# Optimization experiments

Measured on AMD Instinct MI355X. Metric: run time of the kernel, lower is better.

Reference implementation:

```python
import jax, jax.numpy as jnp
import numpy as np

B, S, D_IN = 2, 2048, 1024
DIM, H, G = 64, 16, 4  # head dim, num_heads, kv groups


def setup_inputs() -> dict:
    key = jax.random.key(0)
    ks = jax.random.split(key, 9)
    query = jax.random.normal(ks[0], (B, S, D_IN), dtype=jnp.float32)
    key_t = jax.random.normal(ks[1], (B, S, D_IN), dtype=jnp.float32)
    value = jax.random.normal(ks[2], (B, S, D_IN), dtype=jnp.float32)
    # causal mask; masked_fill where mask == 0
    mask = jnp.tril(jnp.ones((S, S), dtype=jnp.int32))[None]  # [1,S,S]
    sc = 1.0 / np.sqrt(D_IN)
    Wq = jax.random.normal(ks[3], (H, D_IN, DIM), dtype=jnp.float32) * sc
    bq = jnp.zeros((H, DIM), dtype=jnp.float32)
    Wk = jax.random.normal(ks[4], (G, D_IN, DIM), dtype=jnp.float32) * sc
    bk = jnp.zeros((G, DIM), dtype=jnp.float32)
    Wv = jax.random.normal(ks[5], (G, D_IN, DIM), dtype=jnp.float32) * sc
    bv = jnp.zeros((G, DIM), dtype=jnp.float32)
    return {"query": query, "key": key_t, "value": value, "mask": mask,
            "Wq": Wq, "bq": bq, "Wk": Wk, "bk": bk, "Wv": Wv, "bv": bv}


def reference(query, key, value, mask, Wq, bq, Wk, bk, Wv, bv):
    # batched per-head projections (replaces the Python loop over heads)
    Q = jnp.einsum('bsd,hde->bhse', query, Wq) + bq[None, :, None, :]   # [B,H,S,E]
    K = jnp.einsum('bsd,gde->bgse', key, Wk) + bk[None, :, None, :]     # [B,G,S,E]
    V = jnp.einsum('bsd,gde->bgse', value, Wv) + bv[None, :, None, :]   # [B,G,S,E]
    # head i uses KV group i % G (as in the original loop)
    g_idx = jnp.arange(H) % G
    Kh = K[:, g_idx]  # [B,H,S,E]
    Vh = V[:, g_idx]
    attn = jnp.einsum('bhqe,bhke->bhqk', Q, Kh) / np.sqrt(DIM)          # [B,H,S,S]
    attn = jnp.where(mask[:, None] == 0, jnp.float32(-1e9), attn)
    p = jax.nn.softmax(attn, axis=-1)
    z = jnp.einsum('bhqk,bhke->bhqe', p, Vh)                             # [B,H,S,E]
    # concat heads along last dim (same order as torch.cat of z_list)
    return z.transpose(0, 2, 1, 3).reshape(B, S, H * DIM)
```

## Files before the change

### kernel.cpp

```cpp
#include <hip/hip_runtime.h>
#include <hip/hip_bf16.h>
#include <math.h>

#define S_LEN 2048
#define DIN   1024
#define NH    16
#define NG    4

typedef short s16x8 __attribute__((ext_vector_type(8)));
typedef float f32x4 __attribute__((ext_vector_type(4)));

__device__ __forceinline__ unsigned short f2bf(float x) {
  union { float f; unsigned u; } v; v.f = x;
  unsigned r = v.u + 0x7FFFu + ((v.u >> 16) & 1u);
  return (unsigned short)(r >> 16);
}
__device__ __forceinline__ unsigned cvtpk(float a, float b) {
  unsigned r;
  asm("v_cvt_pk_bf16_f32 %0, %1, %2" : "=v"(r) : "v"(a), "v"(b));
  return r;
}

#define GLOAD_LDS16(gsrc, ldst)                                              \
  __builtin_amdgcn_global_load_lds(                                         \
      (const __attribute__((address_space(1))) unsigned int*)(gsrc),        \
      (__attribute__((address_space(3))) unsigned int*)(ldst), 16, 0, 0)


__global__ __launch_bounds__(256) void k_cast(
    const float* __restrict__ q, const float* __restrict__ k,
    const float* __restrict__ v, unsigned short* __restrict__ AF) {
  __shared__ __align__(16) unsigned short L[16][264];
  const int i = blockIdx.y;
  const float* src = (i == 0) ? q : (i == 1) ? k : v;
  unsigned short* dst = AF + (size_t)i * 4194304;
  const int x = blockIdx.x;
  const int b = x >> 9, s16 = (x >> 2) & 127, dblk = x & 3;
  const int t = threadIdx.x;
  const float* base = src + ((size_t)(b * 2048 + s16 * 16)) * 1024 + dblk * 256;

  #pragma unroll
  for (int c = 0; c < 4; ++c) {
    const int idx = c * 256 + t;
    const int row = idx >> 6, c4 = (idx & 63) * 4;
    float4 xv = *(const float4*)(base + (size_t)row * 1024 + c4);
    *(uint2*)&L[row][c4] = make_uint2(cvtpk(xv.x, xv.y), cvtpk(xv.z, xv.w));
  }
  __syncthreads();

  const int w = t >> 6, l = t & 63;
  const int row = l & 15, kk = l >> 4;
  #pragma unroll
  for (int p = 0; p < 2; ++p) {
    const int dk = w * 2 + p;
    const s16x8 vreg = *(const s16x8*)&L[row][dk * 32 + kk * 8];
    unsigned short* op = dst
        + (size_t)((b * 128 + s16) * 32 + dblk * 8 + dk) * 512 + l * 8;
    *(s16x8*)op = vreg;
  }
}

__global__ __launch_bounds__(256) void k_wtrans(
    const float* __restrict__ Wq, const float* __restrict__ Wk,
    const float* __restrict__ Wv, unsigned short* __restrict__ WF) {
  __shared__ __align__(16) unsigned short T[64][72];
  const int u = blockIdx.x >> 4, D0 = (blockIdx.x & 15) * 64;
  const int t = threadIdx.x;
  const float* src = (u < 16) ? (Wq + (size_t)u * 65536)
                   : (u < 20) ? (Wk + (size_t)(u - 16) * 65536)
                              : (Wv + (size_t)(u - 20) * 65536);
  const int e4 = (t & 15) * 4, dl = t >> 4;
  #pragma unroll
  for (int p = 0; p < 4; ++p) {
    const int d = p * 16 + dl;
    float4 v = *(const float4*)(src + (size_t)(D0 + d) * 64 + e4);
    T[e4 + 0][d] = f2bf(v.x); T[e4 + 1][d] = f2bf(v.y);
    T[e4 + 2][d] = f2bf(v.z); T[e4 + 3][d] = f2bf(v.w);
  }
  __syncthreads();
  const int j = t & 7;
  #pragma unroll
  for (int p = 0; p < 2; ++p) {
    const int e = p * 32 + (t >> 3);
    unsigned short* dst = WF + (size_t)u * 65536
        + (size_t)((e >> 4) * 32 + (D0 >> 5) + (j >> 2)) * 512
        + (e & 15) * 8 + (j & 3) * 128;
    *(s16x8*)dst = *(const s16x8*)&T[e][j * 8];
  }
}

__global__ __launch_bounds__(256, 4) void k_project(
    const unsigned short* __restrict__ AF,
    const float* __restrict__ bq, const float* __restrict__ bk,
    const float* __restrict__ bv,
    const unsigned short* __restrict__ WF,
    unsigned short* __restrict__ QF,
    unsigned short* __restrict__ KF,
    unsigned short* __restrict__ VF) {
  const int i = blockIdx.x;
  const int lid = (i & 7) * 96 + (i >> 3);
  const int strip = lid / 48;
  const int rr = lid % 48;
  const int b = rr / 24, u = rr % 24;
  const int tid = threadIdx.x;
  const int w = tid >> 6, lane = tid & 63, lq = lane & 15, gq = lane >> 4;

  const unsigned short* AFp = AF
      + (size_t)((u < 16) ? 0 : (u < 20) ? 1 : 2) * 4194304
      + (size_t)b * 2097152;
  const float* bias = (u < 16) ? bq + u * 64
                    : (u < 20) ? bk + (u - 16) * 64 : bv + (u - 20) * 64;
  const unsigned short* WFp = WF + (size_t)u * 65536;
  const int sb0 = strip * 8 + w * 2;
  const float OSC = (u < 16) ? 0.1803368801111204f : 1.0f;

  f32x4 acc[2][4] = {};
  s16x8 aE[2], bE[4], aO[2], bO[4];

  auto LD = [&](s16x8 (&a)[2], s16x8 (&bf)[4], int dk) {
    a[0] = *(const s16x8*)(AFp + (size_t)((sb0 + 0) * 32 + dk) * 512 + lane * 8);
    a[1] = *(const s16x8*)(AFp + (size_t)((sb0 + 1) * 32 + dk) * 512 + lane * 8);
    #pragma unroll
    for (int n = 0; n < 4; ++n)
      bf[n] = *(const s16x8*)(WFp + (size_t)(n * 32 + dk) * 512 + lane * 8);
  };
  auto FM = [&](const s16x8 (&a)[2], const s16x8 (&bf)[4]) {
    #pragma unroll
    for (int rf = 0; rf < 2; ++rf)
      #pragma unroll
      for (int n = 0; n < 4; ++n)
        acc[rf][n] = __builtin_amdgcn_mfma_f32_16x16x32_bf16(a[rf], bf[n], acc[rf][n], 0, 0, 0);
  };

  LD(aE, bE, 0);
  for (int dk = 0; dk < 32; dk += 2) {
    LD(aO, bO, dk + 1);
    FM(aE, bE);
    if (dk + 2 < 32) LD(aE, bE, dk + 2);
    FM(aO, bO);
  }

  float bvv[4];
  #pragma unroll
  for (int n = 0; n < 4; ++n) bvv[n] = bias[n * 16 + lq];

  unsigned short* dst = (u < 16) ? QF + (size_t)(b * 16 + u) * 131072
                      : (u < 20) ? KF + (size_t)(b * 4 + (u - 16)) * 131072
                                 : VF + (size_t)(b * 4 + (u - 20)) * 131072;
  #pragma unroll
  for (int rf = 0; rf < 2; ++rf)
    #pragma unroll
    for (int n = 0; n < 4; ++n)
      #pragma unroll
      for (int r = 0; r < 4; ++r) {
        const int s = strip * 128 + w * 32 + rf * 16 + gq * 4 + r;
        const int d = n * 16 + lq;
        const unsigned short hv = f2bf((acc[rf][n][r] + bvv[n]) * OSC);
        if (u < 20)
          dst[(size_t)((s >> 4) * 2 + (d >> 5)) * 512
              + (s & 15) * 8 + ((d >> 3) & 3) * 128 + (d & 7)] = hv;
        else
          dst[(size_t)(n * 64 + (s >> 5)) * 512
              + lq * 8 + ((s >> 3) & 3) * 128 + (s & 7)] = hv;
      }
}

__global__ __launch_bounds__(256) void k_attn(
    const unsigned short* __restrict__ QF, const unsigned short* __restrict__ KF,
    const unsigned short* __restrict__ VF, float* __restrict__ out) {
  __shared__ __align__(16) unsigned short KV[2][8192];
  __shared__ __align__(16) unsigned short P[4][16][72];
  const int tid = threadIdx.x;
  const int w = tid >> 6, lane = tid & 63, lq = lane & 15, gq = lane >> 4;
  const int x = blockIdx.x;
  const int xcd = x & 7, li = x >> 3;
  const int g = xcd & 3;
  const int j = 127 - (li * 2 + (xcd >> 2));
  const int h = g + 4 * w;
  const int b = blockIdx.y;

  const unsigned short* QFp = QF + (size_t)(b * NH + h) * 131072;
  const unsigned short* KFp = KF + (size_t)(b * NG + g) * 131072;
  const unsigned short* VFp = VF + (size_t)(b * NG + g) * 131072;
  const int nt = (j >> 2) + 1;

  const s16x8 qf0 = *(const s16x8*)(QFp + (size_t)(j * 2 + 0) * 512 + lane * 8);
  const s16x8 qf1 = *(const s16x8*)(QFp + (size_t)(j * 2 + 1) * 512 + lane * 8);
  f32x4 z[4] = {};
  float lsum = 0.f;

  auto stage = [&](int t, int buf) {
    const unsigned short* ks = KFp + (size_t)t * 4096 + (w * 2) * 512 + lane * 8;
    unsigned short* kd = &KV[buf][(w * 2) * 512];
    GLOAD_LDS16(ks, kd);
    GLOAD_LDS16(ks + 512, kd + 512);
    const unsigned short* vs = VFp + (size_t)(w * 64 + t * 2) * 512 + lane * 8;
    unsigned short* vd = &KV[buf][4096 + (w * 2) * 512];
    GLOAD_LDS16(vs, vd);
    GLOAD_LDS16(vs + 512, vd + 512);
  };

  auto tile = [&](int t, int buf) {
    const unsigned short* kb = &KV[buf][0];
    const unsigned short* vb = &KV[buf][4096];
    f32x4 sv[4];
    __builtin_amdgcn_s_setprio(1);
    #pragma unroll
    for (int f = 0; f < 4; ++f) {
      const s16x8 kA = *(const s16x8*)(kb + (f * 2 + 0) * 512 + lane * 8);
      const s16x8 kB = *(const s16x8*)(kb + (f * 2 + 1) * 512 + lane * 8);
      f32x4 s = {};
      s = __builtin_amdgcn_mfma_f32_16x16x32_bf16(kA, qf0, s, 0, 0, 0);
      s = __builtin_amdgcn_mfma_f32_16x16x32_bf16(kB, qf1, s, 0, 0, 0);
      sv[f] = s;
    }
    __builtin_amdgcn_s_setprio(0);
    if (t == nt - 1) {
      const int k0 = t * 64;
      const int qrow = j * 16 + lq;
      #pragma unroll
      for (int f = 0; f < 4; ++f)
        #pragma unroll
        for (int r = 0; r < 4; ++r)
          if (k0 + f * 16 + gq * 4 + r > qrow) sv[f][r] = -1e30f;
    }
    float s0 = 0.f, s1 = 0.f;
    #pragma unroll
    for (int f = 0; f < 4; ++f) {
      float p0 = __builtin_amdgcn_exp2f(sv[f][0]);
      float p1 = __builtin_amdgcn_exp2f(sv[f][1]);
      float p2 = __builtin_amdgcn_exp2f(sv[f][2]);
      float p3 = __builtin_amdgcn_exp2f(sv[f][3]);
      s0 += p0 + p1; s1 += p2 + p3;
      *(uint2*)&P[w][lq][f * 16 + gq * 4] = make_uint2(cvtpk(p0, p1), cvtpk(p2, p3));
    }
    lsum += s0 + s1;
    const s16x8 pa0 = *(const s16x8*)&P[w][lq][gq * 8];
    const s16x8 pa1 = *(const s16x8*)&P[w][lq][32 + gq * 8];
    __builtin_amdgcn_s_setprio(1);
    #pragma unroll
    for (int n = 0; n < 4; ++n) {
      const s16x8 v0 = *(const s16x8*)(vb + (n * 2 + 0) * 512 + lane * 8);
      const s16x8 v1 = *(const s16x8*)(vb + (n * 2 + 1) * 512 + lane * 8);
      z[n] = __builtin_amdgcn_mfma_f32_16x16x32_bf16(pa0, v0, z[n], 0, 0, 0);
      z[n] = __builtin_amdgcn_mfma_f32_16x16x32_bf16(pa1, v1, z[n], 0, 0, 0);
    }
    __builtin_amdgcn_s_setprio(0);
  };

  stage(0, 0);
  asm volatile("s_waitcnt vmcnt(0)");
  __syncthreads();
  int buf = 0;
  for (int t = 0; t < nt; ++t) {
    if (t + 1 < nt) stage(t + 1, buf ^ 1);
    tile(t, buf);
    asm volatile("s_waitcnt vmcnt(0)");
    __syncthreads();
    buf ^= 1;
  }

  lsum += __shfl_xor(lsum, 16);
  lsum += __shfl_xor(lsum, 32);
  float* outp = out + (size_t)b * S_LEN * 1024 + h * 64;
  #pragma unroll
  for (int r = 0; r < 4; ++r) {
    float lr = __shfl(lsum, gq * 4 + r, 64);
    float inv = __builtin_amdgcn_rcpf(lr);
    float* op = outp + (size_t)(j * 16 + gq * 4 + r) * 1024;
    #pragma unroll
    for (int n = 0; n < 4; ++n) op[n * 16 + lq] = z[n][r] * inv;
  }
}

extern "C" void kernel_launch(void* const* d_in, const int* in_sizes, int n_in,
                              void* d_out, int out_size, void* d_ws, size_t ws_size,
                              hipStream_t stream) {
  const float* query = (const float*)d_in[0];
  const float* key   = (const float*)d_in[1];
  const float* value = (const float*)d_in[2];
  const float* Wq = (const float*)d_in[4];
  const float* bq = (const float*)d_in[5];
  const float* Wk = (const float*)d_in[6];
  const float* bk = (const float*)d_in[7];
  const float* Wv = (const float*)d_in[8];
  const float* bv = (const float*)d_in[9];
  float* out = (float*)d_out;

  unsigned short* AF = (unsigned short*)d_ws;
  unsigned short* WF = AF + 12582912;
  unsigned short* QF = WF + 1572864;
  unsigned short* KF = QF + 4194304;
  unsigned short* VF = KF + 1048576;

  hipLaunchKernelGGL(k_cast, dim3(1024, 3), dim3(256), 0, stream,
                     query, key, value, AF);
  hipLaunchKernelGGL(k_wtrans, dim3(384), dim3(256), 0, stream, Wq, Wk, Wv, WF);
  hipLaunchKernelGGL(k_project, dim3(768), dim3(256), 0, stream,
                     AF, bq, bk, bv, WF, QF, KF, VF);
  hipLaunchKernelGGL(k_attn, dim3(512, 2), dim3(256), 0, stream, QF, KF, VF, out);
}
```

Baseline: 81.14 us.

## Stage projection GEMM operands through double-buffered LDS with direct global-to-LDS loads

The projection kernel now loads its A and W fragments with global_load_lds into double-buffered shared memory, and prefetches the next k-slice while the current one is computed. Previously each wave loaded its own copy of the W fragments straight from global memory into registers. With staging, the four waves share one W copy per block, which cuts redundant global and L2 traffic. The cost is an extra LDS round trip, a block-wide barrier each iteration, and removal of the min-blocks launch bound hint, which may change occupancy.

```diff
diff --git a/kernel.cpp b/kernel.cpp
--- a/kernel.cpp
+++ b/kernel.cpp
@@ -89,7 +89,7 @@
   }
 }
 
-__global__ __launch_bounds__(256, 4) void k_project(
+__global__ __launch_bounds__(256) void k_project(
     const unsigned short* __restrict__ AF,
     const float* __restrict__ bq, const float* __restrict__ bk,
     const float* __restrict__ bv,
@@ -97,6 +97,8 @@
     unsigned short* __restrict__ QF,
     unsigned short* __restrict__ KF,
     unsigned short* __restrict__ VF) {
+  __shared__ __align__(16) unsigned short As[2][8][2][512];
+  __shared__ __align__(16) unsigned short Ws[2][4][2][512];
   const int i = blockIdx.x;
   const int lid = (i & 7) * 96 + (i >> 3);
   const int strip = lid / 48;
@@ -111,33 +113,52 @@
   const float* bias = (u < 16) ? bq + u * 64
                     : (u < 20) ? bk + (u - 16) * 64 : bv + (u - 20) * 64;
   const unsigned short* WFp = WF + (size_t)u * 65536;
-  const int sb0 = strip * 8 + w * 2;
   const float OSC = (u < 16) ? 0.1803368801111204f : 1.0f;
 
+  auto stage = [&](int s, int buf) {
+    const int dk = 2 * s;
+    #pragma unroll
+    for (int p2 = 0; p2 < 2; ++p2) {
+      const int tb = w * 2 + p2;
+      #pragma unroll
+      for (int p = 0; p < 2; ++p) {
+        const unsigned short* src =
+            AFp + (size_t)((strip * 8 + tb) * 32 + dk + p) * 512 + lane * 8;
+        GLOAD_LDS16(src, &As[buf][tb][p][0]);
+      }
+    }
+    #pragma unroll
+    for (int p = 0; p < 2; ++p) {
+      const unsigned short* src =
+          WFp + (size_t)(w * 32 + dk + p) * 512 + lane * 8;
+      GLOAD_LDS16(src, &Ws[buf][w][p][0]);
+    }
+  };
+
   f32x4 acc[2][4] = {};
-  s16x8 aE[2], bE[4], aO[2], bO[4];
-
-  auto LD = [&](s16x8 (&a)[2], s16x8 (&bf)[4], int dk) {
-    a[0] = *(const s16x8*)(AFp + (size_t)((sb0 + 0) * 32 + dk) * 512 + lane * 8);
-    a[1] = *(const s16x8*)(AFp + (size_t)((sb0 + 1) * 32 + dk) * 512 + lane * 8);
-    #pragma unroll
-    for (int n = 0; n < 4; ++n)
-      bf[n] = *(const s16x8*)(WFp + (size_t)(n * 32 + dk) * 512 + lane * 8);
-  };
-  auto FM = [&](const s16x8 (&a)[2], const s16x8 (&bf)[4]) {
-    #pragma unroll
-    for (int rf = 0; rf < 2; ++rf)
+  stage(0, 0);
+  asm volatile("s_waitcnt vmcnt(0)");
+  __syncthreads();
+  int buf = 0;
+  for (int s = 0; s < 16; ++s) {
+    if (s + 1 < 16) stage(s + 1, buf ^ 1);
+    #pragma unroll
+    for (int p = 0; p < 2; ++p) {
+      const s16x8 a0 = *(const s16x8*)&As[buf][w * 2 + 0][p][lane * 8];
+      const s16x8 a1 = *(const s16x8*)&As[buf][w * 2 + 1][p][lane * 8];
+      s16x8 bf[4];
       #pragma unroll
       for (int n = 0; n < 4; ++n)
-        acc[rf][n] = __builtin_amdgcn_mfma_f32_16x16x32_bf16(a[rf], bf[n], acc[rf][n], 0, 0, 0);
-  };
-
-  LD(aE, bE, 0);
-  for (int dk = 0; dk < 32; dk += 2) {
-    LD(aO, bO, dk + 1);
-    FM(aE, bE);
-    if (dk + 2 < 32) LD(aE, bE, dk + 2);
-    FM(aO, bO);
+        bf[n] = *(const s16x8*)&Ws[buf][n][p][lane * 8];
+      #pragma unroll
+      for (int n = 0; n < 4; ++n) {
+        acc[0][n] = __builtin_amdgcn_mfma_f32_16x16x32_bf16(a0, bf[n], acc[0][n], 0, 0, 0);
+        acc[1][n] = __builtin_amdgcn_mfma_f32_16x16x32_bf16(a1, bf[n], acc[1][n], 0, 0, 0);
+      }
+    }
+    asm volatile("s_waitcnt vmcnt(0)");
+    __syncthreads();
+    buf ^= 1;
   }
 
   float bvv[4];
```

After: 81.44 us. About the same (+0.4%).
